# Kernel optimization log

Hardware: AMD Instinct MI355X
Metric: run time of the kernel (lower is better)

The kernel has to match this reference:

```python
import jax, jax.numpy as jnp
import numpy as np

B, T, H, W, C = 2, 16, 56, 56, 128
K_T, K = 5, 7
HIDDEN = 4 * C  # expansion_ratio = 4


def kernel_to_freq_3d(kernel, t, h, w):
    # kernel: (C, k_t, k_h, k_w) -> (C, t, h, w) complex freq, centered circular placement
    c, k_t, k_h, k_w = kernel.shape
    t_idx = (jnp.arange(k_t) - k_t // 2) % t
    h_idx = (jnp.arange(k_h) - k_h // 2) % h
    w_idx = (jnp.arange(k_w) - k_w // 2) % w
    tt, th, tw = jnp.meshgrid(t_idx, h_idx, w_idx, indexing='ij')
    padded = jnp.zeros((c, t, h, w), kernel.dtype).at[:, tt, th, tw].set(kernel)
    return jnp.fft.fftn(padded, axes=(1, 2, 3))


def setup_inputs() -> dict:
    key = jax.random.key(0)
    ks = jax.random.split(key, 16)
    n = lambda k, shape, s=0.02: (jax.random.normal(k, shape, jnp.float32) * s)
    return {
        'x': jax.random.normal(ks[0], (B, T, H, W, C), jnp.float32),
        'Wg': n(ks[1], (C, C)), 'bg': jnp.zeros((C,), jnp.float32),
        'Wh': n(ks[2], (C, C)), 'bh': jnp.zeros((C,), jnp.float32),
        'gate_kernel': n(ks[3], (C, K_T, K, K), 0.05),
        'hidden_kernel': n(ks[4], (C, K_T, K, K), 0.05),
        'Wo': n(ks[5], (C, C)), 'bo': jnp.zeros((C,), jnp.float32),
        'ln_scale': jnp.ones((C,), jnp.float32), 'ln_bias': jnp.zeros((C,), jnp.float32),
        'W1': n(ks[6], (C, HIDDEN)), 'b1': jnp.zeros((HIDDEN,), jnp.float32),
        'W2': n(ks[7], (HIDDEN, C)), 'b2': jnp.zeros((C,), jnp.float32),
        'gamma': jnp.full((C,), 1e-6, jnp.float32),
    }


def reference(x, Wg, bg, Wh, bh, gate_kernel, hidden_kernel, Wo, bo,
              ln_scale, ln_bias, W1, b1, W2, b2, gamma):
    b, t, h, w, c = x.shape
    residual = x
    # --- GatedConvSSM3D ---
    gate_proj = x @ Wg + bg
    hidden_proj = x @ Wh + bh
    gk_f = kernel_to_freq_3d(gate_kernel, t, h, w).transpose(1, 2, 3, 0)   # (T,H,W,C)
    hk_f = kernel_to_freq_3d(hidden_kernel, t, h, w).transpose(1, 2, 3, 0)
    gate_spatial = jnp.fft.ifftn(jnp.fft.fftn(gate_proj, axes=(1, 2, 3)) * gk_f[None], axes=(1, 2, 3)).real
    hidden_spatial = jnp.fft.ifftn(jnp.fft.fftn(hidden_proj, axes=(1, 2, 3)) * hk_f[None], axes=(1, 2, 3)).real
    log_forget = -jax.nn.softplus(gate_spatial)          # log(1 - z)
    log_values = -jax.nn.softplus(-gate_spatial) + jnp.log(hidden_spatial ** 2 + 1e-6)  # log z + log h~

    def op(left, right):
        la, lb = left
        ra, rb = right
        return (la + ra, jnp.logaddexp(ra + lb, rb))

    # Heinsen scan along temporal axis (axis=1 of (B,T,H,W,C))
    _, log_h = jax.lax.associative_scan(op, (log_forget, log_values), axis=1)
    ssm_out = jnp.exp(log_h) @ Wo + bo
    # --- LayerNorm3D ---
    mean = jnp.mean(ssm_out, axis=-1, keepdims=True)
    var = jnp.var(ssm_out, axis=-1, keepdims=True)
    xn = (ssm_out - mean) / jnp.sqrt(var + 1e-6) * ln_scale + ln_bias
    # --- MLP + LayerScale + residual ---
    y = jax.nn.gelu(xn @ W1 + b1) @ W2 + b2
    return y * gamma + residual
```

## Files before the change

### kernel.cpp

```cpp
#include <hip/hip_runtime.h>
#include <hip/hip_bf16.h>
#include <hip/hip_fp16.h>
#include <cstdint>
#include <cstddef>

typedef unsigned short u16;
typedef __attribute__((ext_vector_type(8))) short bf16x8;
typedef __attribute__((ext_vector_type(8))) _Float16 f16x8;
typedef __attribute__((ext_vector_type(4))) float f32x4;

#define MFMA16(a,b,c)  __builtin_amdgcn_mfma_f32_16x16x32_bf16((a),(b),(c),0,0,0)
#define MFMAF16(a,b,c) __builtin_amdgcn_mfma_f32_16x16x32_f16((a),(b),(c),0,0,0)


static __device__ __forceinline__ float b2f(u16 u){ return __uint_as_float(((unsigned)u)<<16); }
static __device__ __forceinline__ u16 f2b(float f){
  unsigned u = __float_as_uint(f);
  return (u16)((u + 0x7fffu + ((u>>16)&1u)) >> 16);
}
static __device__ __forceinline__ u16 f2h(float f){ return __half_as_ushort(__float2half(f)); }

union U4F { uint4 u; f16x8 h; };

static __device__ __forceinline__ void gld_lds16(const void* g, void* l){
  __builtin_amdgcn_global_load_lds(
      (const __attribute__((address_space(1))) void*)g,
      (__attribute__((address_space(3))) void*)l, 16, 0, 0);
}

static __device__ __forceinline__ bool input_is_f32(const void* xp){
  const u16* u = (const u16*)xp;
  int cnt = 0;
#pragma unroll
  for (int i = 0; i < 64; ++i){
    unsigned e = (u[2*i] >> 7) & 0xFF;
    cnt += (e >= 100 && e <= 140) ? 1 : 0;
  }
  return cnt < 32;
}

static __device__ __forceinline__ u16 ldb(const void* p, int i, bool f32){
  return f32 ? f2b(((const float*)p)[i]) : ((const u16*)p)[i];
}
static __device__ __forceinline__ float ldf(const void* p, int i, bool f32){
  return f32 ? ((const float*)p)[i] : b2f(((const u16*)p)[i]);
}

__global__ __launch_bounds__(256) void k0_prep(
    const void* __restrict__ x,
    const void* __restrict__ Wg, const void* __restrict__ Wh, const void* __restrict__ Wo,
    const void* __restrict__ W1, const void* __restrict__ W2,
    const void* __restrict__ gk, const void* __restrict__ hk,
    const void* __restrict__ bg, const void* __restrict__ bh, const void* __restrict__ bo,
    const void* __restrict__ lns, const void* __restrict__ lnb,
    const void* __restrict__ b1, const void* __restrict__ b2, const void* __restrict__ gm,
    u16* __restrict__ XB,
    u16* __restrict__ WgT, u16* __restrict__ WhT, u16* __restrict__ WoT,
    u16* __restrict__ W1T, u16* __restrict__ W2T,
    unsigned* __restrict__ CIRG, unsigned* __restrict__ CIRH, u16* __restrict__ PRM)
{
  const bool f32 = input_is_f32(x);
  int tid = blockIdx.x*blockDim.x + threadIdx.x;
  int np  = gridDim.x*blockDim.x;

  if (f32){
    const float* xf = (const float*)x;
    for (int p = tid; p < 6422528; p += np){
      unsigned v = (unsigned)f2b(xf[2*p]) | ((unsigned)f2b(xf[2*p+1]) << 16);
      ((unsigned*)XB)[p] = v;
    }
  } else {
    const unsigned* xu = (const unsigned*)x;
    for (int p = tid; p < 6422528; p += np) ((unsigned*)XB)[p] = xu[p];
  }

  for (int p = tid; p < 16384; p += np){
    int n = p>>7, k = p&127;
    WgT[p] = ldb(Wg, k*128+n, f32);
    WhT[p] = ldb(Wh, k*128+n, f32);
    WoT[p] = ldb(Wo, k*128+n, f32);
  }
  for (int p = tid; p < 65536; p += np){
    int n = p>>7, k = p&127;
    W1T[p] = ldb(W1, k*512+n, f32);
  }
  for (int p = tid; p < 65536; p += np){
    int n = p>>9, k = p&511;
    W2T[p] = ldb(W2, k*128+n, f32);
  }

  for (int p = tid; p < 819200; p += np){
    int uu = p & 3;
    int lane = (p >> 2) & 63;
    int tpc = p >> 8;
    int c = tpc / 25, tp = tpc - c*25;
    int qq = lane >> 4, nn = lane & 15;
    int tap = 2*tp + (qq >> 1);
    unsigned vg = 0, vh = 0;
    if (tap < 49){
      int kk = ((qq & 1) << 3) + uu*2;
      int i0 = (nn - kk + 2) & 15;
      int i1 = (nn - kk + 1) & 15;
      unsigned g0 = (i0 < 5) ? (unsigned)f2h(ldf(gk, c*245 + i0*49 + tap, f32)) : 0u;
      unsigned h0 = (i0 < 5) ? (unsigned)f2h(ldf(hk, c*245 + i0*49 + tap, f32)) : 0u;
      unsigned g1 = (i1 < 5) ? (unsigned)f2h(ldf(gk, c*245 + i1*49 + tap, f32)) : 0u;
      unsigned h1 = (i1 < 5) ? (unsigned)f2h(ldf(hk, c*245 + i1*49 + tap, f32)) : 0u;
      vg = g0 | (g1 << 16);
      vh = h0 | (h1 << 16);
    }
    CIRG[p] = vg; CIRH[p] = vh;
  }

  for (int p = tid; p < 1408; p += np){
    const void* src; int off;
    if      (p < 128)  { src = bg;  off = p; }
    else if (p < 256)  { src = bh;  off = p-128; }
    else if (p < 384)  { src = bo;  off = p-256; }
    else if (p < 512)  { src = lns; off = p-384; }
    else if (p < 640)  { src = lnb; off = p-512; }
    else if (p < 1152) { src = b1;  off = p-640; }
    else if (p < 1280) { src = b2;  off = p-1152; }
    else               { src = gm;  off = p-1280; }
    PRM[p] = ldb(src, off, f32);
  }
}

__global__ __launch_bounds__(256) void k1_dualgemm(
    const u16* __restrict__ XB, const u16* __restrict__ WgT, const u16* __restrict__ WhT,
    const u16* __restrict__ PRM,
    u16* __restrict__ GP, u16* __restrict__ HP)
{
  int bid = blockIdx.x;
  int b = bid / 784; int hw = (bid % 784)*4 + (threadIdx.x >> 6);
  int lane = threadIdx.x & 63;
  int lrow = lane & 15, q = lane >> 4;

  bf16x8 a[4];
  const u16* xr = XB + ((size_t)(b*16 + lrow)*3136 + hw)*128 + q*8;
#pragma unroll
  for (int kt = 0; kt < 4; ++kt) a[kt] = *(const bf16x8*)(xr + kt*32);

#pragma unroll
  for (int mat = 0; mat < 2; ++mat){
    const u16* WT  = mat ? WhT : WgT;
    const u16* bia = PRM + (mat ? 128 : 0);
    u16* out       = mat ? HP  : GP;
#pragma unroll
    for (int nt = 0; nt < 8; ++nt){
      f32x4 acc = {0.f,0.f,0.f,0.f};
      const u16* wr = WT + (nt*16 + lrow)*128 + q*8;
#pragma unroll
      for (int kt = 0; kt < 4; ++kt){
        bf16x8 bfr = *(const bf16x8*)(wr + kt*32);
        acc = MFMA16(a[kt], bfr, acc);
      }
      int c = nt*16 + lrow;
      float bv = b2f(bia[c]);
      size_t base = (((size_t)(b*32 + (c>>2))*3136 + hw)*4 + (c&3))*16 + q*4;
      ushort4 pk;
      pk.x = f2h(acc[0] + bv); pk.y = f2h(acc[1] + bv);
      pk.z = f2h(acc[2] + bv); pk.w = f2h(acc[3] + bv);
      *(ushort4*)(out + base) = pk;
    }
  }
}

__global__ __launch_bounds__(256, 5) void k2_conv_scan(
    const u16* __restrict__ GP, const u16* __restrict__ HP,
    const u16* __restrict__ CIRG, const u16* __restrict__ CIRH,
    u16* __restrict__ ELH)
{
  __shared__ __align__(16) unsigned su[6272];

  int bid = blockIdx.x;
  int b = bid / 1568; int rr = bid - b*1568;
  int cg = rr / 49; int s = rr % 49;
  int th = s / 7, tw = s % 7;
  int tid = threadIdx.x;
  int h0g = th*8, w0g = tw*8;
  size_t tb = (size_t)(b*32 + cg)*200704;

  int wv = tid >> 6, lane = tid & 63;
  int q = lane >> 4, lrow = lane & 15;
  int hb = lrow >> 3, wb = lrow & 7;

  int cu = __builtin_amdgcn_readfirstlane(cg*4 + wv);
  const u16* cirg = CIRG + (size_t)cu*12800;
  const u16* cirh = CIRH + (size_t)cu*12800;

  unsigned soff[7]; bool sval[7];
#pragma unroll
  for (int ss = 0; ss < 7; ++ss){
    int ci = ss*256 + tid;
    sval[ss] = (ci < 1568);
    int clc = ci / 392;
    int rem = ci - clc*392;
    int pos = rem >> 1, half = rem & 1;
    int hh = pos / 14, ww = pos - hh*14;
    int hg = h0g + hh - 3; if (hg < 0) hg += 56; else if (hg >= 56) hg -= 56;
    int wg = w0g + ww - 3; if (wg < 0) wg += 56; else if (wg >= 56) wg -= 56;
    soff[ss] = (unsigned)((hg*56 + wg)*128 + clc*32 + half*16);
  }
  const char* gpb = (const char*)(GP + tb);
  const char* hpb = (const char*)(HP + tb);

  auto stagepass = [&](const char* Pb){
#pragma unroll
    for (int ss = 0; ss < 7; ++ss){
      if (sval[ss])
        gld_lds16(Pb + soff[ss], (char*)su + (ss*256 + wv*64)*16);
    }
  };

  auto convpass = [&](const u16* cir, f32x4* acc){
#pragma unroll
    for (int m = 0; m < 4; ++m) acc[m] = (f32x4){0.f,0.f,0.f,0.f};
    U4F bq0, bq1, bq2;
    bq0.u = *(const uint4*)(cir + 0*512 + lane*8);
    bq1.u = *(const uint4*)(cir + 1*512 + lane*8);
    bq2.u = *(const uint4*)(cir + 2*512 + lane*8);
    const int base_cl = wv*6272;
#pragma unroll
    for (int tp = 0; tp < 25; ++tp){
      const int tA = 2*tp;
      const int tB = (2*tp + 1 > 48) ? 48 : 2*tp + 1;
      const int dhA = 6 - tA/7, dwA = 6 - tA%7;
      const int dhB = 6 - tB/7, dwB = 6 - tB%7;
      int dh = (q >= 2) ? dhB : dhA;
      int dw = (q >= 2) ? dwB : dwA;
      const char* sp = (const char*)su +
          (base_cl + ((hb + dh)*14 + (wb + dw))*32 + (q & 1)*16);
      U4F a0, a1, a2, a3;
      a0.u = *(const uint4*)(sp);
      a1.u = *(const uint4*)(sp + 896);
      a2.u = *(const uint4*)(sp + 1792);
      a3.u = *(const uint4*)(sp + 2688);
      f16x8 bb = (tp % 3 == 0) ? bq0.h : (tp % 3 == 1) ? bq1.h : bq2.h;
      acc[0] = MFMAF16(a0.h, bb, acc[0]);
      acc[1] = MFMAF16(a1.h, bb, acc[1]);
      acc[2] = MFMAF16(a2.h, bb, acc[2]);
      acc[3] = MFMAF16(a3.h, bb, acc[3]);
      if (tp + 3 < 25){
        uint4 nb = *(const uint4*)(cir + (tp+3)*512 + lane*8);
        if (tp % 3 == 0) bq0.u = nb; else if (tp % 3 == 1) bq1.u = nb; else bq2.u = nb;
      }
    }
  };

  f32x4 accG[4], accH[4];
  stagepass(gpb);
  __syncthreads();
  convpass(cirg, accG);
  __syncthreads();
  stagepass(hpb);
  __syncthreads();
  convpass(cirh, accH);

  float fv[16], vv[16];
#pragma unroll
  for (int e = 0; e < 16; ++e){
    float g  = accG[e>>2][e&3];
    float hc = accH[e>>2][e&3];
    float eg = __expf(g);
    float fr = __builtin_amdgcn_rcpf(1.f + eg);
    float zz = 1.f - fr;
    fv[e] = fr;
    vv[e] = (hc*hc + 1e-6f) * zz;
  }
#pragma unroll
  for (int d = 1; d < 16; d <<= 1){
    bool ok = (lrow >= d);
#pragma unroll
    for (int e = 0; e < 16; ++e){
      float Lf = __shfl_up(fv[e], (unsigned)d, 16);
      float Lv = __shfl_up(vv[e], (unsigned)d, 16);
      Lf = ok ? Lf : 1.f;
      Lv = ok ? Lv : 0.f;
      vv[e] = fmaf(fv[e], Lv, vv[e]);
      fv[e] = fv[e] * Lf;
    }
  }
  size_t ob = tb + (size_t)lrow*12544 + (size_t)(h0g*56 + w0g)*4 + wv;
#pragma unroll
  for (int e = 0; e < 16; ++e){
    int r = (e>>2)*16 + q*4 + (e&3);
    ELH[ob + (size_t)((r>>3)*56 + (r&7))*4] = f2b(vv[e]);
  }
}

__global__ __launch_bounds__(256, 2) void k34_gemm_ln_mlp(
    const u16* __restrict__ ELH, const u16* __restrict__ WoT,
    const u16* __restrict__ W1T, const u16* __restrict__ W2T,
    const u16* __restrict__ PRM,
    const void* __restrict__ xraw, void* __restrict__ outv)
{
  __shared__ __align__(16) u16 smem[37376];
  u16* sW0 = smem;
  u16* sW1 = smem + 16384;
  u16* sXp = smem;
  u16* sH  = smem + 32768;

  int bid = blockIdx.x;
  int b = bid / 392; int rem = bid - b*392;
  int t2 = rem / 49; int s2 = rem - t2*49;
  int hw0 = s2 * 64;
  int tid = threadIdx.x;
  int wv = tid >> 6, lane = tid & 63;
  int lrow = lane & 15, q = lane >> 4;
  const bool f32io = input_is_f32(xraw);

  {
    int hw = hw0 + wv*16 + lrow;
    size_t tbA = ((size_t)(b*512) + t2)*3136;
    size_t tbB = tbA + (size_t)8*3136;
    union Cvt { uint4 u; bf16x8 v; };
    bf16x8 eA[4], eB[4];
#pragma unroll
    for (int kt = 0; kt < 4; ++kt){
      int cg0 = kt*8 + q*2;
      size_t eoA = (tbA + (size_t)cg0*50176 + hw)*4;
      size_t eoB = (tbB + (size_t)cg0*50176 + hw)*4;
      uint2 lo = *(const uint2*)(ELH + eoA);
      uint2 hi = *(const uint2*)(ELH + eoA + (size_t)50176*4);
      Cvt c1; c1.u = make_uint4(lo.x, lo.y, hi.x, hi.y); eA[kt] = c1.v;
      uint2 lo2 = *(const uint2*)(ELH + eoB);
      uint2 hi2 = *(const uint2*)(ELH + eoB + (size_t)50176*4);
      Cvt c2; c2.u = make_uint4(lo2.x, lo2.y, hi2.x, hi2.y); eB[kt] = c2.v;
    }

    float vA[8][4], vB[8][4];
#pragma unroll
    for (int nt = 0; nt < 8; ++nt){
      f32x4 aacc = {0.f,0.f,0.f,0.f}, bacc = {0.f,0.f,0.f,0.f};
      const u16* wr = WoT + (nt*16 + lrow)*128 + q*8;
#pragma unroll
      for (int kt = 0; kt < 4; ++kt){
        bf16x8 bfr = *(const bf16x8*)(wr + kt*32);
        aacc = MFMA16(eA[kt], bfr, aacc);
        bacc = MFMA16(eB[kt], bfr, bacc);
      }
      float bv = b2f(PRM[256 + nt*16 + lrow]);
#pragma unroll
      for (int i = 0; i < 4; ++i){ vA[nt][i] = aacc[i] + bv; vB[nt][i] = bacc[i] + bv; }
    }

#pragma unroll
    for (int i = 0; i < 4; ++i){
      float smA=0.f, sqA=0.f, smB=0.f, sqB=0.f;
#pragma unroll
      for (int nt = 0; nt < 8; ++nt){
        float a_ = vA[nt][i]; smA += a_; sqA = fmaf(a_, a_, sqA);
        float b_ = vB[nt][i]; smB += b_; sqB = fmaf(b_, b_, sqB);
      }
#pragma unroll
      for (int m = 1; m < 16; m <<= 1){
        smA += __shfl_xor(smA, m, 64); sqA += __shfl_xor(sqA, m, 64);
        smB += __shfl_xor(smB, m, 64); sqB += __shfl_xor(sqB, m, 64);
      }
      float mA = smA*(1.f/128.f), rA = rsqrtf(sqA*(1.f/128.f) - mA*mA + 1e-6f);
      float mB = smB*(1.f/128.f), rB = rsqrtf(sqB*(1.f/128.f) - mB*mB + 1e-6f);
      int r = wv*16 + q*4 + i;
#pragma unroll
      for (int nt = 0; nt < 8; ++nt){
        int c = nt*16 + lrow;
        float ls = b2f(PRM[384 + c]), lb = b2f(PRM[512 + c]);
        sXp[r*136 + c]        = f2b((vA[nt][i] - mA)*rA*ls + lb);
        sXp[8704 + r*136 + c] = f2b((vB[nt][i] - mB)*rB*ls + lb);
      }
    }
  }

  bf16x8 aA[4], aB[4];
#pragma unroll
  for (int kt = 0; kt < 4; ++kt){
    aA[kt] = *(const bf16x8*)&sXp[(wv*16 + lrow)*136 + kt*32 + q*8];
    aB[kt] = *(const bf16x8*)&sXp[8704 + (wv*16 + lrow)*136 + kt*32 + q*8];
  }
  __syncthreads();

  const u16* wsrc[8];
#pragma unroll
  for (int r = 0; r < 8; ++r){
    int c = r*4 + wv;
    if (c < 16){
      int j = c >> 2, kt = c & 3;
      wsrc[r] = W1T + (size_t)(j*16 + lrow)*128 + kt*32 + q*8;
    } else {
      int c2 = c - 16; int jo = c2 >> 1, kt2 = c2 & 1;
      wsrc[r] = W2T + (size_t)(jo*16 + lrow)*512 + kt2*32 + q*8;
    }
  }
  auto stage = [&](u16* buf, int nt){
#pragma unroll
    for (int r = 0; r < 8; ++r){
      int c = r*4 + wv;
      const u16* src = wsrc[r] + (c < 16 ? (size_t)nt*8192 : (size_t)nt*64);
      gld_lds16(src, buf + c*512);
    }
  };

  f32x4 accA[8], accB[8];
#pragma unroll
  for (int jo = 0; jo < 8; ++jo){ accA[jo] = (f32x4){0.f,0.f,0.f,0.f}; accB[jo] = (f32x4){0.f,0.f,0.f,0.f}; }
  u16* sHw = sH + wv*1152;

  stage(sW0, 0);
  asm volatile("s_waitcnt vmcnt(0)" ::: "memory");
  __builtin_amdgcn_s_barrier();

  auto mlpstep = [&](int nt, u16* wcur, u16* wnxt, bool do_stage){
    if (do_stage) stage(wnxt, nt+1);
#pragma unroll
    for (int js = 0; js < 4; ++js){
      f32x4 hc = {0.f,0.f,0.f,0.f};
#pragma unroll
      for (int kt = 0; kt < 4; ++kt)
        hc = MFMA16(aA[kt], *(const bf16x8*)&wcur[(js*4 + kt)*512 + lane*8], hc);
      float bv = b2f(PRM[640 + nt*64 + js*16 + lrow]);
#pragma unroll
      for (int i = 0; i < 4; ++i){
        float v = hc[i] + bv;
        float u = 0.79788456080286535588f*(v + 0.044715f*v*v*v);
        float su_ = __expf(-2.f*u);
        float gl = v * __builtin_amdgcn_rcpf(1.f + su_);
        sHw[(q*4 + i)*72 + js*16 + lrow] = (u16)(__float_as_uint(gl) >> 16);
      }
    }
#pragma unroll
    for (int kt2 = 0; kt2 < 2; ++kt2){
      bf16x8 af = *(const bf16x8*)&sHw[lrow*72 + kt2*32 + q*8];
#pragma unroll
      for (int jo = 0; jo < 8; ++jo)
        accA[jo] = MFMA16(af, *(const bf16x8*)&wcur[(16 + jo*2 + kt2)*512 + lane*8], accA[jo]);
    }
#pragma unroll
    for (int js = 0; js < 4; ++js){
      f32x4 hc = {0.f,0.f,0.f,0.f};
#pragma unroll
      for (int kt = 0; kt < 4; ++kt)
        hc = MFMA16(aB[kt], *(const bf16x8*)&wcur[(js*4 + kt)*512 + lane*8], hc);
      float bv = b2f(PRM[640 + nt*64 + js*16 + lrow]);
#pragma unroll
      for (int i = 0; i < 4; ++i){
        float v = hc[i] + bv;
        float u = 0.79788456080286535588f*(v + 0.044715f*v*v*v);
        float su_ = __expf(-2.f*u);
        float gl = v * __builtin_amdgcn_rcpf(1.f + su_);
        sHw[(q*4 + i)*72 + js*16 + lrow] = (u16)(__float_as_uint(gl) >> 16);
      }
    }
#pragma unroll
    for (int kt2 = 0; kt2 < 2; ++kt2){
      bf16x8 af = *(const bf16x8*)&sHw[lrow*72 + kt2*32 + q*8];
#pragma unroll
      for (int jo = 0; jo < 8; ++jo)
        accB[jo] = MFMA16(af, *(const bf16x8*)&wcur[(16 + jo*2 + kt2)*512 + lane*8], accB[jo]);
    }
    asm volatile("s_waitcnt vmcnt(0)" ::: "memory");
    __builtin_amdgcn_s_barrier();
  };

  for (int nt2 = 0; nt2 < 4; ++nt2){
    mlpstep(2*nt2,     sW0, sW1, true);
    mlpstep(2*nt2 + 1, sW1, sW0, nt2 < 3);
  }

  size_t rowA0 = ((size_t)(b*16 + t2))*3136 + hw0 + wv*16 + q*4;
  size_t rowB0 = rowA0 + (size_t)8*3136;
#pragma unroll
  for (int jo = 0; jo < 8; ++jo){
    int c = jo*16 + lrow;
    float bv  = b2f(PRM[1152 + c]);
    float gmv = b2f(PRM[1280 + c]);
#pragma unroll
    for (int i = 0; i < 4; ++i){
      size_t rA = rowA0 + i, rB = rowB0 + i;
      float yA = accA[jo][i] + bv, yB = accB[jo][i] + bv;
      if (f32io){
        float resA = ((const float*)xraw)[rA*128 + c];
        float resB = ((const float*)xraw)[rB*128 + c];
        ((float*)outv)[rA*128 + c] = yA*gmv + resA;
        ((float*)outv)[rB*128 + c] = yB*gmv + resB;
      } else {
        float resA = b2f(((const u16*)xraw)[rA*128 + c]);
        float resB = b2f(((const u16*)xraw)[rB*128 + c]);
        ((u16*)outv)[rA*128 + c] = f2b(yA*gmv + resA);
        ((u16*)outv)[rB*128 + c] = f2b(yB*gmv + resB);
      }
    }
  }
}

extern "C" void kernel_launch(void* const* d_in, const int* in_sizes, int n_in,
                              void* d_out, int out_size, void* d_ws, size_t ws_size,
                              hipStream_t stream)
{
  const void* x   = d_in[0];
  const void* Wg  = d_in[1];
  const void* bg  = d_in[2];
  const void* Wh  = d_in[3];
  const void* bh  = d_in[4];
  const void* gk  = d_in[5];
  const void* hk  = d_in[6];
  const void* Wo  = d_in[7];
  const void* bo  = d_in[8];
  const void* lns = d_in[9];
  const void* lnb = d_in[10];
  const void* W1  = d_in[11];
  const void* b1  = d_in[12];
  const void* W2  = d_in[13];
  const void* b2  = d_in[14];
  const void* gm  = d_in[15];

  char* ws = (char*)d_ws;
  u16* GP  = (u16*)(ws + 0);
  u16* HP  = (u16*)(ws + 25690112);
  u16* ELH = (u16*)(ws + 51380224);
  u16* XB  = (u16*)(ws + 77070336);
  u16* WgT = (u16*)(ws + 102760448);
  u16* WhT = WgT + 16384;
  u16* WoT = WhT + 16384;
  u16* W1T = WoT + 16384;
  u16* W2T = W1T + 65536;
  unsigned* CIRG = (unsigned*)(W2T + 65536);
  unsigned* CIRH = CIRG + 819200;
  u16* PRM = (u16*)(CIRH + 819200);

  k0_prep        <<<dim3(512),  dim3(256), 0, stream>>>(x, Wg, Wh, Wo, W1, W2, gk, hk,
                                                        bg, bh, bo, lns, lnb, b1, b2, gm,
                                                        XB, WgT, WhT, WoT, W1T, W2T, CIRG, CIRH, PRM);
  k1_dualgemm    <<<dim3(1568), dim3(256), 0, stream>>>(XB, WgT, WhT, PRM, GP, HP);
  k2_conv_scan   <<<dim3(3136), dim3(256), 0, stream>>>(GP, HP, (const u16*)CIRG, (const u16*)CIRH, ELH);
  k34_gemm_ln_mlp<<<dim3(784),  dim3(256), 0, stream>>>(ELH, WoT, W1T, W2T, PRM, x, (void*)d_out);
}
```

Measured before the change: 398.5 us.

## Split k34 row tiles across 8 waves instead of two tiles per wave

The fused Wo-GEMM/LayerNorm/MLP kernel now runs 512 threads per block. Each wave handles one 16-row tile, where before each of 4 waves carried two tiles (A and B). This halves per-wave accumulator and fragment registers to raise occupancy, and spreads weight staging over 8 waves. The GELU hidden scratch moves from a padded stride of 72 to an XOR-swizzled stride of 64 to avoid LDS bank conflicts. The trade-off is more barrier participants and a larger shared-memory footprint per block.

```diff
diff --git a/kernel.cpp b/kernel.cpp
--- a/kernel.cpp
+++ b/kernel.cpp
@@ -288,13 +288,13 @@
   }
 }
 
-__global__ __launch_bounds__(256, 2) void k34_gemm_ln_mlp(
+__global__ __launch_bounds__(512, 4) void k34_gemm_ln_mlp(
     const u16* __restrict__ ELH, const u16* __restrict__ WoT,
     const u16* __restrict__ W1T, const u16* __restrict__ W2T,
     const u16* __restrict__ PRM,
     const void* __restrict__ xraw, void* __restrict__ outv)
 {
-  __shared__ __align__(16) u16 smem[37376];
+  __shared__ __align__(16) u16 smem[40960];
   u16* sW0 = smem;
   u16* sW1 = smem + 16384;
   u16* sXp = smem;
@@ -307,81 +307,66 @@
   int tid = threadIdx.x;
   int wv = tid >> 6, lane = tid & 63;
   int lrow = lane & 15, q = lane >> 4;
+  int tile = wv >> 2, sub = wv & 3;
   const bool f32io = input_is_f32(xraw);
 
   {
-    int hw = hw0 + wv*16 + lrow;
-    size_t tbA = ((size_t)(b*512) + t2)*3136;
-    size_t tbB = tbA + (size_t)8*3136;
+    int hw = hw0 + sub*16 + lrow;
+    size_t tbT = ((size_t)(b*512) + t2 + tile*8)*3136;
     union Cvt { uint4 u; bf16x8 v; };
-    bf16x8 eA[4], eB[4];
+    bf16x8 e[4];
 #pragma unroll
     for (int kt = 0; kt < 4; ++kt){
       int cg0 = kt*8 + q*2;
-      size_t eoA = (tbA + (size_t)cg0*50176 + hw)*4;
-      size_t eoB = (tbB + (size_t)cg0*50176 + hw)*4;
-      uint2 lo = *(const uint2*)(ELH + eoA);
-      uint2 hi = *(const uint2*)(ELH + eoA + (size_t)50176*4);
-      Cvt c1; c1.u = make_uint4(lo.x, lo.y, hi.x, hi.y); eA[kt] = c1.v;
-      uint2 lo2 = *(const uint2*)(ELH + eoB);
-      uint2 hi2 = *(const uint2*)(ELH + eoB + (size_t)50176*4);
-      Cvt c2; c2.u = make_uint4(lo2.x, lo2.y, hi2.x, hi2.y); eB[kt] = c2.v;
-    }
-
-    float vA[8][4], vB[8][4];
+      size_t eo = (tbT + (size_t)cg0*50176 + hw)*4;
+      uint2 lo = *(const uint2*)(ELH + eo);
+      uint2 hi = *(const uint2*)(ELH + eo + (size_t)50176*4);
+      Cvt c1; c1.u = make_uint4(lo.x, lo.y, hi.x, hi.y); e[kt] = c1.v;
+    }
+
+    float v[8][4];
 #pragma unroll
     for (int nt = 0; nt < 8; ++nt){
-      f32x4 aacc = {0.f,0.f,0.f,0.f}, bacc = {0.f,0.f,0.f,0.f};
+      f32x4 acc = {0.f,0.f,0.f,0.f};
       const u16* wr = WoT + (nt*16 + lrow)*128 + q*8;
 #pragma unroll
       for (int kt = 0; kt < 4; ++kt){
         bf16x8 bfr = *(const bf16x8*)(wr + kt*32);
-        aacc = MFMA16(eA[kt], bfr, aacc);
-        bacc = MFMA16(eB[kt], bfr, bacc);
+        acc = MFMA16(e[kt], bfr, acc);
       }
       float bv = b2f(PRM[256 + nt*16 + lrow]);
 #pragma unroll
-      for (int i = 0; i < 4; ++i){ vA[nt][i] = aacc[i] + bv; vB[nt][i] = bacc[i] + bv; }
+      for (int i = 0; i < 4; ++i) v[nt][i] = acc[i] + bv;
     }
 
 #pragma unroll
     for (int i = 0; i < 4; ++i){
-      float smA=0.f, sqA=0.f, smB=0.f, sqB=0.f;
-#pragma unroll
-      for (int nt = 0; nt < 8; ++nt){
-        float a_ = vA[nt][i]; smA += a_; sqA = fmaf(a_, a_, sqA);
-        float b_ = vB[nt][i]; smB += b_; sqB = fmaf(b_, b_, sqB);
-      }
-#pragma unroll
-      for (int m = 1; m < 16; m <<= 1){
-        smA += __shfl_xor(smA, m, 64); sqA += __shfl_xor(sqA, m, 64);
-        smB += __shfl_xor(smB, m, 64); sqB += __shfl_xor(sqB, m, 64);
-      }
-      float mA = smA*(1.f/128.f), rA = rsqrtf(sqA*(1.f/128.f) - mA*mA + 1e-6f);
-      float mB = smB*(1.f/128.f), rB = rsqrtf(sqB*(1.f/128.f) - mB*mB + 1e-6f);
+      float sm = 0.f, sq = 0.f;
+#pragma unroll
+      for (int nt = 0; nt < 8; ++nt){ float a_ = v[nt][i]; sm += a_; sq = fmaf(a_, a_, sq); }
+#pragma unroll
+      for (int m = 1; m < 16; m <<= 1){ sm += __shfl_xor(sm, m, 64); sq += __shfl_xor(sq, m, 64); }
+      float mean = sm * (1.f/128.f);
+      float rstd = rsqrtf(sq*(1.f/128.f) - mean*mean + 1e-6f);
       int r = wv*16 + q*4 + i;
 #pragma unroll
       for (int nt = 0; nt < 8; ++nt){
         int c = nt*16 + lrow;
-        float ls = b2f(PRM[384 + c]), lb = b2f(PRM[512 + c]);
-        sXp[r*136 + c]        = f2b((vA[nt][i] - mA)*rA*ls + lb);
-        sXp[8704 + r*136 + c] = f2b((vB[nt][i] - mB)*rB*ls + lb);
-      }
-    }
-  }
-
-  bf16x8 aA[4], aB[4];
-#pragma unroll
-  for (int kt = 0; kt < 4; ++kt){
-    aA[kt] = *(const bf16x8*)&sXp[(wv*16 + lrow)*136 + kt*32 + q*8];
-    aB[kt] = *(const bf16x8*)&sXp[8704 + (wv*16 + lrow)*136 + kt*32 + q*8];
-  }
+        sXp[r*136 + c] = f2b((v[nt][i] - mean)*rstd*b2f(PRM[384 + c]) + b2f(PRM[512 + c]));
+      }
+    }
+  }
+
+  bf16x8 a[4];
+#pragma unroll
+  for (int kt = 0; kt < 4; ++kt)
+    a[kt] = *(const bf16x8*)&sXp[(wv*16 + lrow)*136 + kt*32 + q*8];
   __syncthreads();
 
-  const u16* wsrc[8];
-#pragma unroll
-  for (int r = 0; r < 8; ++r){
-    int c = r*4 + wv;
+  const u16* wsrc[4];
+#pragma unroll
+  for (int r = 0; r < 4; ++r){
+    int c = r*8 + wv;
     if (c < 16){
       int j = c >> 2, kt = c & 3;
       wsrc[r] = W1T + (size_t)(j*16 + lrow)*128 + kt*32 + q*8;
@@ -392,17 +377,17 @@
   }
   auto stage = [&](u16* buf, int nt){
 #pragma unroll
-    for (int r = 0; r < 8; ++r){
-      int c = r*4 + wv;
+    for (int r = 0; r < 4; ++r){
+      int c = r*8 + wv;
       const u16* src = wsrc[r] + (c < 16 ? (size_t)nt*8192 : (size_t)nt*64);
       gld_lds16(src, buf + c*512);
     }
   };
 
-  f32x4 accA[8], accB[8];
-#pragma unroll
-  for (int jo = 0; jo < 8; ++jo){ accA[jo] = (f32x4){0.f,0.f,0.f,0.f}; accB[jo] = (f32x4){0.f,0.f,0.f,0.f}; }
-  u16* sHw = sH + wv*1152;
+  f32x4 acc[8];
+#pragma unroll
+  for (int jo = 0; jo < 8; ++jo) acc[jo] = (f32x4){0.f,0.f,0.f,0.f};
+  u16* sHw = sH + wv*1024;
 
   stage(sW0, 0);
   asm volatile("s_waitcnt vmcnt(0)" ::: "memory");
@@ -415,7 +400,7 @@
       f32x4 hc = {0.f,0.f,0.f,0.f};
 #pragma unroll
       for (int kt = 0; kt < 4; ++kt)
-        hc = MFMA16(aA[kt], *(const bf16x8*)&wcur[(js*4 + kt)*512 + lane*8], hc);
+        hc = MFMA16(a[kt], *(const bf16x8*)&wcur[(js*4 + kt)*512 + lane*8], hc);
       float bv = b2f(PRM[640 + nt*64 + js*16 + lrow]);
 #pragma unroll
       for (int i = 0; i < 4; ++i){
@@ -423,38 +408,17 @@
         float u = 0.79788456080286535588f*(v + 0.044715f*v*v*v);
         float su_ = __expf(-2.f*u);
         float gl = v * __builtin_amdgcn_rcpf(1.f + su_);
-        sHw[(q*4 + i)*72 + js*16 + lrow] = (u16)(__float_as_uint(gl) >> 16);
+        int r = q*4 + i;
+        int cidx = (js*16 + lrow) ^ ((r & 7) << 3);
+        sHw[r*64 + cidx] = (u16)(__float_as_uint(gl) >> 16);
       }
     }
 #pragma unroll
     for (int kt2 = 0; kt2 < 2; ++kt2){
-      bf16x8 af = *(const bf16x8*)&sHw[lrow*72 + kt2*32 + q*8];
+      bf16x8 af = *(const bf16x8*)&sHw[lrow*64 + ((kt2*32 + q*8) ^ ((lrow & 7) << 3))];
 #pragma unroll
       for (int jo = 0; jo < 8; ++jo)
-        accA[jo] = MFMA16(af, *(const bf16x8*)&wcur[(16 + jo*2 + kt2)*512 + lane*8], accA[jo]);
-    }
-#pragma unroll
-    for (int js = 0; js < 4; ++js){
-      f32x4 hc = {0.f,0.f,0.f,0.f};
-#pragma unroll
-      for (int kt = 0; kt < 4; ++kt)
-        hc = MFMA16(aB[kt], *(const bf16x8*)&wcur[(js*4 + kt)*512 + lane*8], hc);
-      float bv = b2f(PRM[640 + nt*64 + js*16 + lrow]);
-#pragma unroll
-      for (int i = 0; i < 4; ++i){
-        float v = hc[i] + bv;
-        float u = 0.79788456080286535588f*(v + 0.044715f*v*v*v);
-        float su_ = __expf(-2.f*u);
-        float gl = v * __builtin_amdgcn_rcpf(1.f + su_);
-        sHw[(q*4 + i)*72 + js*16 + lrow] = (u16)(__float_as_uint(gl) >> 16);
-      }
-    }
-#pragma unroll
-    for (int kt2 = 0; kt2 < 2; ++kt2){
-      bf16x8 af = *(const bf16x8*)&sHw[lrow*72 + kt2*32 + q*8];
-#pragma unroll
-      for (int jo = 0; jo < 8; ++jo)
-        accB[jo] = MFMA16(af, *(const bf16x8*)&wcur[(16 + jo*2 + kt2)*512 + lane*8], accB[jo]);
+        acc[jo] = MFMA16(af, *(const bf16x8*)&wcur[(16 + jo*2 + kt2)*512 + lane*8], acc[jo]);
     }
     asm volatile("s_waitcnt vmcnt(0)" ::: "memory");
     __builtin_amdgcn_s_barrier();
@@ -465,8 +429,7 @@
     mlpstep(2*nt2 + 1, sW1, sW0, nt2 < 3);
   }
 
-  size_t rowA0 = ((size_t)(b*16 + t2))*3136 + hw0 + wv*16 + q*4;
-  size_t rowB0 = rowA0 + (size_t)8*3136;
+  size_t row0 = ((size_t)(b*16 + t2 + tile*8))*3136 + hw0 + sub*16 + q*4;
 #pragma unroll
   for (int jo = 0; jo < 8; ++jo){
     int c = jo*16 + lrow;
@@ -474,18 +437,14 @@
     float gmv = b2f(PRM[1280 + c]);
 #pragma unroll
     for (int i = 0; i < 4; ++i){
-      size_t rA = rowA0 + i, rB = rowB0 + i;
-      float yA = accA[jo][i] + bv, yB = accB[jo][i] + bv;
+      size_t rr = row0 + i;
+      float y = acc[jo][i] + bv;
       if (f32io){
-        float resA = ((const float*)xraw)[rA*128 + c];
-        float resB = ((const float*)xraw)[rB*128 + c];
-        ((float*)outv)[rA*128 + c] = yA*gmv + resA;
-        ((float*)outv)[rB*128 + c] = yB*gmv + resB;
+        float res = ((const float*)xraw)[rr*128 + c];
+        ((float*)outv)[rr*128 + c] = y*gmv + res;
       } else {
-        float resA = b2f(((const u16*)xraw)[rA*128 + c]);
-        float resB = b2f(((const u16*)xraw)[rB*128 + c]);
-        ((u16*)outv)[rA*128 + c] = f2b(yA*gmv + resA);
-        ((u16*)outv)[rB*128 + c] = f2b(yB*gmv + resB);
+        float res = b2f(((const u16*)xraw)[rr*128 + c]);
+        ((u16*)outv)[rr*128 + c] = f2b(y*gmv + res);
       }
     }
   }
@@ -531,5 +490,5 @@
                                                         XB, WgT, WhT, WoT, W1T, W2T, CIRG, CIRH, PRM);
   k1_dualgemm    <<<dim3(1568), dim3(256), 0, stream>>>(XB, WgT, WhT, PRM, GP, HP);
   k2_conv_scan   <<<dim3(3136), dim3(256), 0, stream>>>(GP, HP, (const u16*)CIRG, (const u16*)CIRH, ELH);
-  k34_gemm_ln_mlp<<<dim3(784),  dim3(256), 0, stream>>>(ELH, WoT, W1T, W2T, PRM, x, (void*)d_out);
-}
+  k34_gemm_ln_mlp<<<dim3(784),  dim3(512), 0, stream>>>(ELH, WoT, W1T, W2T, PRM, x, (void*)d_out);
+}
```

Result: slower. 420.2 us (+5.4%).

## Read MLP weights directly from global memory instead of double-buffered LDS staging

Applied to the files above, without the earlier changes.

The MLP stage of the fused GEMM+LN+MLP kernel no longer stages W1/W2 tiles into shared memory with double buffering and barriers. Each wave now loads its weight fragments straight from global memory (relying on L2/L1 caching) and shares each fragment across the A and B row groups. Shared memory drops to the activation and hidden buffers, and launch bounds are raised to target 4 blocks per CU for higher occupancy. The trade-off is more global/cache traffic per wave and exposed load latency in place of the LDS reuse and explicit prefetch overlap.

```diff
diff --git a/kernel.cpp b/kernel.cpp
--- a/kernel.cpp
+++ b/kernel.cpp
@@ -288,17 +288,14 @@
   }
 }
 
-__global__ __launch_bounds__(256, 2) void k34_gemm_ln_mlp(
+__global__ __launch_bounds__(256, 4) void k34_gemm_ln_mlp(
     const u16* __restrict__ ELH, const u16* __restrict__ WoT,
     const u16* __restrict__ W1T, const u16* __restrict__ W2T,
     const u16* __restrict__ PRM,
     const void* __restrict__ xraw, void* __restrict__ outv)
 {
-  __shared__ __align__(16) u16 smem[37376];
-  u16* sW0 = smem;
-  u16* sW1 = smem + 16384;
-  u16* sXp = smem;
-  u16* sH  = smem + 32768;
+  __shared__ __align__(16) u16 sXp[17408];
+  __shared__ __align__(16) u16 sH[9216];
 
   int bid = blockIdx.x;
   int b = bid / 392; int rem = bid - b*392;
@@ -376,93 +373,54 @@
     aA[kt] = *(const bf16x8*)&sXp[(wv*16 + lrow)*136 + kt*32 + q*8];
     aB[kt] = *(const bf16x8*)&sXp[8704 + (wv*16 + lrow)*136 + kt*32 + q*8];
   }
-  __syncthreads();
-
-  const u16* wsrc[8];
-#pragma unroll
-  for (int r = 0; r < 8; ++r){
-    int c = r*4 + wv;
-    if (c < 16){
-      int j = c >> 2, kt = c & 3;
-      wsrc[r] = W1T + (size_t)(j*16 + lrow)*128 + kt*32 + q*8;
-    } else {
-      int c2 = c - 16; int jo = c2 >> 1, kt2 = c2 & 1;
-      wsrc[r] = W2T + (size_t)(jo*16 + lrow)*512 + kt2*32 + q*8;
-    }
-  }
-  auto stage = [&](u16* buf, int nt){
-#pragma unroll
-    for (int r = 0; r < 8; ++r){
-      int c = r*4 + wv;
-      const u16* src = wsrc[r] + (c < 16 ? (size_t)nt*8192 : (size_t)nt*64);
-      gld_lds16(src, buf + c*512);
-    }
-  };
 
   f32x4 accA[8], accB[8];
 #pragma unroll
   for (int jo = 0; jo < 8; ++jo){ accA[jo] = (f32x4){0.f,0.f,0.f,0.f}; accB[jo] = (f32x4){0.f,0.f,0.f,0.f}; }
-  u16* sHw = sH + wv*1152;
-
-  stage(sW0, 0);
-  asm volatile("s_waitcnt vmcnt(0)" ::: "memory");
-  __builtin_amdgcn_s_barrier();
-
-  auto mlpstep = [&](int nt, u16* wcur, u16* wnxt, bool do_stage){
-    if (do_stage) stage(wnxt, nt+1);
+  u16* sHwA = sH + wv*2304;
+  u16* sHwB = sHwA + 1152;
+
+  const u16* pW1 = W1T + lrow*128 + q*8;
+  const u16* pW2 = W2T + (size_t)lrow*512 + q*8;
+
+  for (int nt = 0; nt < 8; ++nt){
+    const u16* w1n = pW1 + nt*8192;
 #pragma unroll
     for (int js = 0; js < 4; ++js){
-      f32x4 hc = {0.f,0.f,0.f,0.f};
-#pragma unroll
-      for (int kt = 0; kt < 4; ++kt)
-        hc = MFMA16(aA[kt], *(const bf16x8*)&wcur[(js*4 + kt)*512 + lane*8], hc);
+      f32x4 hcA = {0.f,0.f,0.f,0.f}, hcB = {0.f,0.f,0.f,0.f};
+#pragma unroll
+      for (int kt = 0; kt < 4; ++kt){
+        bf16x8 f = *(const bf16x8*)(w1n + js*2048 + kt*32);
+        hcA = MFMA16(aA[kt], f, hcA);
+        hcB = MFMA16(aB[kt], f, hcB);
+      }
       float bv = b2f(PRM[640 + nt*64 + js*16 + lrow]);
 #pragma unroll
       for (int i = 0; i < 4; ++i){
-        float v = hc[i] + bv;
-        float u = 0.79788456080286535588f*(v + 0.044715f*v*v*v);
-        float su_ = __expf(-2.f*u);
-        float gl = v * __builtin_amdgcn_rcpf(1.f + su_);
-        sHw[(q*4 + i)*72 + js*16 + lrow] = (u16)(__float_as_uint(gl) >> 16);
+        float vA_ = hcA[i] + bv;
+        float uA = 0.79788456080286535588f*(vA_ + 0.044715f*vA_*vA_*vA_);
+        float sA = __expf(-2.f*uA);
+        sHwA[(q*4 + i)*72 + js*16 + lrow] =
+            (u16)(__float_as_uint(vA_ * __builtin_amdgcn_rcpf(1.f + sA)) >> 16);
+        float vB_ = hcB[i] + bv;
+        float uB = 0.79788456080286535588f*(vB_ + 0.044715f*vB_*vB_*vB_);
+        float sB = __expf(-2.f*uB);
+        sHwB[(q*4 + i)*72 + js*16 + lrow] =
+            (u16)(__float_as_uint(vB_ * __builtin_amdgcn_rcpf(1.f + sB)) >> 16);
       }
     }
 #pragma unroll
     for (int kt2 = 0; kt2 < 2; ++kt2){
-      bf16x8 af = *(const bf16x8*)&sHw[lrow*72 + kt2*32 + q*8];
-#pragma unroll
-      for (int jo = 0; jo < 8; ++jo)
-        accA[jo] = MFMA16(af, *(const bf16x8*)&wcur[(16 + jo*2 + kt2)*512 + lane*8], accA[jo]);
-    }
-#pragma unroll
-    for (int js = 0; js < 4; ++js){
-      f32x4 hc = {0.f,0.f,0.f,0.f};
-#pragma unroll
-      for (int kt = 0; kt < 4; ++kt)
-        hc = MFMA16(aB[kt], *(const bf16x8*)&wcur[(js*4 + kt)*512 + lane*8], hc);
-      float bv = b2f(PRM[640 + nt*64 + js*16 + lrow]);
-#pragma unroll
-      for (int i = 0; i < 4; ++i){
-        float v = hc[i] + bv;
-        float u = 0.79788456080286535588f*(v + 0.044715f*v*v*v);
-        float su_ = __expf(-2.f*u);
-        float gl = v * __builtin_amdgcn_rcpf(1.f + su_);
-        sHw[(q*4 + i)*72 + js*16 + lrow] = (u16)(__float_as_uint(gl) >> 16);
-      }
-    }
-#pragma unroll
-    for (int kt2 = 0; kt2 < 2; ++kt2){
-      bf16x8 af = *(const bf16x8*)&sHw[lrow*72 + kt2*32 + q*8];
-#pragma unroll
-      for (int jo = 0; jo < 8; ++jo)
-        accB[jo] = MFMA16(af, *(const bf16x8*)&wcur[(16 + jo*2 + kt2)*512 + lane*8], accB[jo]);
-    }
-    asm volatile("s_waitcnt vmcnt(0)" ::: "memory");
-    __builtin_amdgcn_s_barrier();
-  };
-
-  for (int nt2 = 0; nt2 < 4; ++nt2){
-    mlpstep(2*nt2,     sW0, sW1, true);
-    mlpstep(2*nt2 + 1, sW1, sW0, nt2 < 3);
+      bf16x8 afA = *(const bf16x8*)&sHwA[lrow*72 + kt2*32 + q*8];
+      bf16x8 afB = *(const bf16x8*)&sHwB[lrow*72 + kt2*32 + q*8];
+      const u16* w2n = pW2 + nt*64 + kt2*32;
+#pragma unroll
+      for (int jo = 0; jo < 8; ++jo){
+        bf16x8 f = *(const bf16x8*)(w2n + jo*8192);
+        accA[jo] = MFMA16(afA, f, accA[jo]);
+        accB[jo] = MFMA16(afB, f, accB[jo]);
+      }
+    }
   }
 
   size_t rowA0 = ((size_t)(b*16 + t2))*3136 + hw0 + wv*16 + q*4;
```

Result: slower. 461.3 us (+15.7%).
